# Performance work log

Measured on AMD Instinct MI355X. Metric: run time of the kernel, lower is better.

Reference implementation:

```python
import jax, jax.numpy as jnp
import numpy as np

B, S, H = 8, 2048, 768
VOCAB, MODAL_V, SEG_V, NPI_V, MAX_POS = 32000, 16, 4, 10000, 2048
LN_EPS = 1e-12


def _sinusoidal_table(max_pos, hidden):
    pos = np.arange(max_pos, dtype=np.float32)[:, None]          # [P,1]
    idx = np.arange(hidden, dtype=np.float32)[None, :]           # [1,H]
    angle = pos / np.power(10000.0, 2.0 * idx / hidden)          # even_code/odd_code share 2*idx/H exponent
    tab = np.where(np.arange(hidden)[None, :] % 2 == 0, np.sin(angle), np.cos(angle))
    return jnp.asarray(tab, dtype=jnp.float32)


def setup_inputs() -> dict:
    key = jax.random.key(0)
    ks = jax.random.split(key, 16)
    inp = {
        'word_ids': jax.random.randint(ks[0], (B, S), 0, VOCAB),
        'modalities_ids': jax.random.randint(ks[1], (B, S), 0, MODAL_V),
        'seg_ids': jax.random.randint(ks[2], (B, S), 0, SEG_V),
        'npi_ids': jax.random.randint(ks[3], (B, S), 0, NPI_V),
        'posi_ids': jnp.sort(jax.random.randint(ks[4], (B, S), 0, MAX_POS), axis=-1),
        'age_tau': jax.random.uniform(ks[5], (B, S), dtype=jnp.float32) * 100.0,
        'delays_tau': jax.random.uniform(ks[6], (B, S), dtype=jnp.float32) * 100.0,
        'word_table': jax.random.normal(ks[7], (VOCAB, H), dtype=jnp.float32) * 0.02,
        'modalities_table': jax.random.normal(ks[8], (MODAL_V, H), dtype=jnp.float32) * 0.02,
        'seg_table': jax.random.normal(ks[9], (SEG_V, H), dtype=jnp.float32) * 0.02,
        'npi_table': jax.random.normal(ks[10], (NPI_V, H), dtype=jnp.float32) * 0.02,
        'posi_table': _sinusoidal_table(MAX_POS, H),
        'age_w': jax.random.normal(ks[11], (1, H - 1), dtype=jnp.float32),
        'age_b': jax.random.normal(ks[12], (H - 1,), dtype=jnp.float32),
        'age_w0': jax.random.normal(ks[13], (1, 1), dtype=jnp.float32),
        'age_b0': jax.random.normal(ks[14], (1,), dtype=jnp.float32),
        'delay_w': jax.random.normal(ks[15], (1, H - 1), dtype=jnp.float32),
        'delay_b': jax.random.normal(jax.random.fold_in(key, 100), (H - 1,), dtype=jnp.float32),
        'delay_w0': jax.random.normal(jax.random.fold_in(key, 101), (1, 1), dtype=jnp.float32),
        'delay_b0': jax.random.normal(jax.random.fold_in(key, 102), (1,), dtype=jnp.float32),
        'ln_gamma': jnp.ones((H,), dtype=jnp.float32),
        'ln_beta': jnp.zeros((H,), dtype=jnp.float32),
    }
    return inp


def _time2vec(tau, w, b, w0, b0):
    # tau: [B,S] scalar times; w: [1,H-1]; w0: [1,1]. Vectorized SineActivation.
    t = tau[..., None]                      # [B,S,1]
    v1 = jnp.sin(t * w[0] + b)              # [B,S,H-1]
    v2 = t * w0[0] + b0                     # [B,S,1]
    return jnp.concatenate([v1, v2], axis=-1)


def _layer_norm(x, gamma, beta, eps):
    mu = jnp.mean(x, axis=-1, keepdims=True)
    var = jnp.mean(jnp.square(x - mu), axis=-1, keepdims=True)
    return (x - mu) * jax.lax.rsqrt(var + eps) * gamma + beta


def reference(word_ids, modalities_ids, seg_ids, npi_ids, posi_ids, age_tau, delays_tau,
              word_table, modalities_table, seg_table, npi_table, posi_table,
              age_w, age_b, age_w0, age_b0, delay_w, delay_b, delay_w0, delay_b0,
              ln_gamma, ln_beta):
    word_e = word_table[word_ids]
    seg_e = seg_table[seg_ids]
    modal_e = modalities_table[modalities_ids]
    npi_e = npi_table[npi_ids]
    posi_e = posi_table[posi_ids]
    age_e = _time2vec(age_tau, age_w, age_b, age_w0, age_b0)
    delay_e = _time2vec(delays_tau, delay_w, delay_b, delay_w0, delay_b0)
    # else-branch: sum of all seven embeddings
    emb = word_e + seg_e + posi_e + modal_e + delay_e + age_e + npi_e
    emb = _layer_norm(emb, ln_gamma, ln_beta, LN_EPS)
    return emb  # dropout is identity in eval mode
```

## Files before the change

kernel.cpp:

```cpp
#include <hip/hip_runtime.h>
#include <cmath>

static constexpr int B_ = 8;
static constexpr int S_ = 2048;
static constexpr int H_ = 768;
static constexpr int TOKENS = B_ * S_;
static constexpr float LN_EPS = 1e-12f;

typedef float nfloat4 __attribute__((ext_vector_type(4)));

__device__ __forceinline__ float rfl_f32(float x) {
    return __uint_as_float(__builtin_amdgcn_readfirstlane(__float_as_uint(x)));
}

__global__ __launch_bounds__(256, 5) void bert_emb_kernel(
    const int* __restrict__ word_ids,
    const int* __restrict__ modal_ids,
    const int* __restrict__ seg_ids,
    const int* __restrict__ npi_ids,
    const int* __restrict__ posi_ids,
    const float* __restrict__ age_tau,
    const float* __restrict__ delay_tau,
    const float* __restrict__ word_table,
    const float* __restrict__ modal_table,
    const float* __restrict__ seg_table,
    const float* __restrict__ npi_table,
    const float* __restrict__ posi_table,
    const float* __restrict__ age_w,
    const float* __restrict__ age_b,
    const float* __restrict__ age_w0,
    const float* __restrict__ age_b0,
    const float* __restrict__ delay_w,
    const float* __restrict__ delay_b,
    const float* __restrict__ delay_w0,
    const float* __restrict__ delay_b0,
    const float* __restrict__ ln_gamma,
    const float* __restrict__ ln_beta,
    float* __restrict__ out)
{
    __shared__ __align__(16) float s_aw[H_];
    __shared__ __align__(16) float s_ab[H_];
    __shared__ __align__(16) float s_dw[H_];
    __shared__ __align__(16) float s_db[H_];
    __shared__ __align__(16) float s_g [H_];
    __shared__ __align__(16) float s_bt[H_];

    for (int i = threadIdx.x; i < H_; i += 256) {
        const bool in = (i < H_ - 1);
        s_aw[i] = in ? age_w[i]   : 0.0f;
        s_ab[i] = in ? age_b[i]   : 0.0f;
        s_dw[i] = in ? delay_w[i] : 0.0f;
        s_db[i] = in ? delay_b[i] : 0.0f;
        s_g [i] = ln_gamma[i];
        s_bt[i] = ln_beta[i];
    }
    __syncthreads();

    const int wave = threadIdx.x >> 6;
    const int lane = threadIdx.x & 63;
    const int token = (blockIdx.x << 2) + wave;

    const int wid = __builtin_amdgcn_readfirstlane(word_ids[token]);
    const int mid = __builtin_amdgcn_readfirstlane(modal_ids[token]);
    const int sid = __builtin_amdgcn_readfirstlane(seg_ids[token]);
    const int nid = __builtin_amdgcn_readfirstlane(npi_ids[token]);
    const int pid = __builtin_amdgcn_readfirstlane(posi_ids[token]);
    const float atau = rfl_f32(age_tau[token]);
    const float dtau = rfl_f32(delay_tau[token]);
    const float aw0 = age_w0[0], ab0 = age_b0[0];
    const float dw0 = delay_w0[0], db0 = delay_b0[0];

    const float4* wrow = reinterpret_cast<const float4*>(word_table  + (size_t)wid * H_);
    const float4* mrow = reinterpret_cast<const float4*>(modal_table + (size_t)mid * H_);
    const float4* srow = reinterpret_cast<const float4*>(seg_table   + (size_t)sid * H_);
    const float4* nrow = reinterpret_cast<const float4*>(npi_table   + (size_t)nid * H_);
    const float4* prow = reinterpret_cast<const float4*>(posi_table  + (size_t)pid * H_);

    const float4 w0 = wrow[lane], w1 = wrow[lane + 64], w2 = wrow[lane + 128];
    const float4 m0 = mrow[lane], m1 = mrow[lane + 64], m2 = mrow[lane + 128];
    const float4 s0 = srow[lane], s1 = srow[lane + 64], s2 = srow[lane + 128];
    const float4 n0 = nrow[lane], n1 = nrow[lane + 64], n2 = nrow[lane + 128];
    const float4 p0 = prow[lane], p1 = prow[lane + 64], p2 = prow[lane + 128];

    const float4* awv = reinterpret_cast<const float4*>(s_aw);
    const float4* abv = reinterpret_cast<const float4*>(s_ab);
    const float4* dwv = reinterpret_cast<const float4*>(s_dw);
    const float4* dbv = reinterpret_cast<const float4*>(s_db);

    float vals[12];
    float ssum = 0.0f, ssq = 0.0f;

    const float4 wcs[3] = {w0, w1, w2};
    const float4 mcs[3] = {m0, m1, m2};
    const float4 scs[3] = {s0, s1, s2};
    const float4 ncs[3] = {n0, n1, n2};
    const float4 pcs[3] = {p0, p1, p2};

#pragma unroll
    for (int c = 0; c < 3; ++c) {
        const int h4 = lane + (c << 6);
        const float4 we = wcs[c];
        const float4 me = mcs[c];
        const float4 se = scs[c];
        const float4 ne = ncs[c];
        const float4 pe = pcs[c];

        const float4 aw = awv[h4];
        const float4 ab = abv[h4];
        const float4 dw = dwv[h4];
        const float4 db = dbv[h4];

        float av0 = __sinf(atau * aw.x + ab.x);
        float av1 = __sinf(atau * aw.y + ab.y);
        float av2 = __sinf(atau * aw.z + ab.z);
        float av3 = __sinf(atau * aw.w + ab.w);
        float dv0 = __sinf(dtau * dw.x + db.x);
        float dv1 = __sinf(dtau * dw.y + db.y);
        float dv2 = __sinf(dtau * dw.z + db.z);
        float dv3 = __sinf(dtau * dw.w + db.w);
        if (h4 == (H_ / 4 - 1)) {
            av3 = atau * aw0 + ab0;
            dv3 = dtau * dw0 + db0;
        }

        const float e0 = we.x + me.x + se.x + ne.x + pe.x + av0 + dv0;
        const float e1 = we.y + me.y + se.y + ne.y + pe.y + av1 + dv1;
        const float e2 = we.z + me.z + se.z + ne.z + pe.z + av2 + dv2;
        const float e3 = we.w + me.w + se.w + ne.w + pe.w + av3 + dv3;

        vals[c * 4 + 0] = e0;
        vals[c * 4 + 1] = e1;
        vals[c * 4 + 2] = e2;
        vals[c * 4 + 3] = e3;
        ssum += e0 + e1 + e2 + e3;
        ssq  += e0 * e0 + e1 * e1 + e2 * e2 + e3 * e3;
    }

#pragma unroll
    for (int off = 32; off > 0; off >>= 1) {
        ssum += __shfl_down(ssum, off);
        ssq  += __shfl_down(ssq,  off);
    }
    ssum = __shfl(ssum, 0);
    ssq  = __shfl(ssq,  0);

    const float inv_h = 1.0f / (float)H_;
    const float mu = ssum * inv_h;
    const float var = ssq * inv_h - mu * mu;
    const float rstd = rsqrtf(var + LN_EPS);

    const float4* gv = reinterpret_cast<const float4*>(s_g);
    const float4* bv = reinterpret_cast<const float4*>(s_bt);
    nfloat4* orow = reinterpret_cast<nfloat4*>(out + (size_t)token * H_);

#pragma unroll
    for (int c = 0; c < 3; ++c) {
        const int h4 = lane + (c << 6);
        const float4 g  = gv[h4];
        const float4 bt = bv[h4];
        nfloat4 o;
        o.x = (vals[c * 4 + 0] - mu) * rstd * g.x + bt.x;
        o.y = (vals[c * 4 + 1] - mu) * rstd * g.y + bt.y;
        o.z = (vals[c * 4 + 2] - mu) * rstd * g.z + bt.z;
        o.w = (vals[c * 4 + 3] - mu) * rstd * g.w + bt.w;
        __builtin_nontemporal_store(o, &orow[h4]);
    }
}

extern "C" void kernel_launch(void* const* d_in, const int* in_sizes, int n_in,
                              void* d_out, int out_size, void* d_ws, size_t ws_size,
                              hipStream_t stream) {
    const int*   word_ids    = (const int*)  d_in[0];
    const int*   modal_ids   = (const int*)  d_in[1];
    const int*   seg_ids     = (const int*)  d_in[2];
    const int*   npi_ids     = (const int*)  d_in[3];
    const int*   posi_ids    = (const int*)  d_in[4];
    const float* age_tau     = (const float*)d_in[5];
    const float* delay_tau   = (const float*)d_in[6];
    const float* word_table  = (const float*)d_in[7];
    const float* modal_table = (const float*)d_in[8];
    const float* seg_table   = (const float*)d_in[9];
    const float* npi_table   = (const float*)d_in[10];
    const float* posi_table  = (const float*)d_in[11];
    const float* age_w       = (const float*)d_in[12];
    const float* age_b       = (const float*)d_in[13];
    const float* age_w0      = (const float*)d_in[14];
    const float* age_b0      = (const float*)d_in[15];
    const float* delay_w     = (const float*)d_in[16];
    const float* delay_b     = (const float*)d_in[17];
    const float* delay_w0    = (const float*)d_in[18];
    const float* delay_b0    = (const float*)d_in[19];
    const float* ln_gamma    = (const float*)d_in[20];
    const float* ln_beta     = (const float*)d_in[21];
    float* out = (float*)d_out;

    dim3 grid(TOKENS / 4);
    dim3 block(256);
    hipLaunchKernelGGL(bert_emb_kernel, grid, block, 0, stream,
                       word_ids, modal_ids, seg_ids, npi_ids, posi_ids,
                       age_tau, delay_tau,
                       word_table, modal_table, seg_table, npi_table, posi_table,
                       age_w, age_b, age_w0, age_b0,
                       delay_w, delay_b, delay_w0, delay_b0,
                       ln_gamma, ln_beta, out);
}
```

Measured before the change: 231.2 us.

## Vectorize smem staging, stage gather loads, raise occupancy bound, use xor reduction

Raises the launch-bounds occupancy hint from 5 to 6 blocks per CU. Shared-memory parameter staging now uses one float4 per thread instead of scalar loops. Gathers of the third row chunk are deferred until after the first chunk is consumed, which cuts live registers. The LayerNorm reduction switches to an xor butterfly that removes the final broadcast shuffles. The risk is that fewer loads in flight per wave reduce memory-level parallelism in this bandwidth-bound gather kernel.

```diff
diff --git a/kernel.cpp b/kernel.cpp
--- a/kernel.cpp
+++ b/kernel.cpp
@@ -13,7 +13,7 @@
     return __uint_as_float(__builtin_amdgcn_readfirstlane(__float_as_uint(x)));
 }
 
-__global__ __launch_bounds__(256, 5) void bert_emb_kernel(
+__global__ __launch_bounds__(256, 6) void bert_emb_kernel(
     const int* __restrict__ word_ids,
     const int* __restrict__ modal_ids,
     const int* __restrict__ seg_ids,
@@ -45,14 +45,26 @@
     __shared__ __align__(16) float s_g [H_];
     __shared__ __align__(16) float s_bt[H_];
 
-    for (int i = threadIdx.x; i < H_; i += 256) {
-        const bool in = (i < H_ - 1);
-        s_aw[i] = in ? age_w[i]   : 0.0f;
-        s_ab[i] = in ? age_b[i]   : 0.0f;
-        s_dw[i] = in ? delay_w[i] : 0.0f;
-        s_db[i] = in ? delay_b[i] : 0.0f;
-        s_g [i] = ln_gamma[i];
-        s_bt[i] = ln_beta[i];
+    if (threadIdx.x < 192) {
+        const int i4 = threadIdx.x;
+        float4 vaw, vab, vdw, vdb;
+        if (i4 < 191) {
+            vaw = reinterpret_cast<const float4*>(age_w)[i4];
+            vab = reinterpret_cast<const float4*>(age_b)[i4];
+            vdw = reinterpret_cast<const float4*>(delay_w)[i4];
+            vdb = reinterpret_cast<const float4*>(delay_b)[i4];
+        } else {
+            vaw = make_float4(age_w[764],   age_w[765],   age_w[766],   0.0f);
+            vab = make_float4(age_b[764],   age_b[765],   age_b[766],   0.0f);
+            vdw = make_float4(delay_w[764], delay_w[765], delay_w[766], 0.0f);
+            vdb = make_float4(delay_b[764], delay_b[765], delay_b[766], 0.0f);
+        }
+        reinterpret_cast<float4*>(s_aw)[i4] = vaw;
+        reinterpret_cast<float4*>(s_ab)[i4] = vab;
+        reinterpret_cast<float4*>(s_dw)[i4] = vdw;
+        reinterpret_cast<float4*>(s_db)[i4] = vdb;
+        reinterpret_cast<float4*>(s_g )[i4] = reinterpret_cast<const float4*>(ln_gamma)[i4];
+        reinterpret_cast<float4*>(s_bt)[i4] = reinterpret_cast<const float4*>(ln_beta)[i4];
     }
     __syncthreads();
 
@@ -76,12 +88,6 @@
     const float4* nrow = reinterpret_cast<const float4*>(npi_table   + (size_t)nid * H_);
     const float4* prow = reinterpret_cast<const float4*>(posi_table  + (size_t)pid * H_);
 
-    const float4 w0 = wrow[lane], w1 = wrow[lane + 64], w2 = wrow[lane + 128];
-    const float4 m0 = mrow[lane], m1 = mrow[lane + 64], m2 = mrow[lane + 128];
-    const float4 s0 = srow[lane], s1 = srow[lane + 64], s2 = srow[lane + 128];
-    const float4 n0 = nrow[lane], n1 = nrow[lane + 64], n2 = nrow[lane + 128];
-    const float4 p0 = prow[lane], p1 = prow[lane + 64], p2 = prow[lane + 128];
-
     const float4* awv = reinterpret_cast<const float4*>(s_aw);
     const float4* abv = reinterpret_cast<const float4*>(s_ab);
     const float4* dwv = reinterpret_cast<const float4*>(s_dw);
@@ -90,21 +96,9 @@
     float vals[12];
     float ssum = 0.0f, ssq = 0.0f;
 
-    const float4 wcs[3] = {w0, w1, w2};
-    const float4 mcs[3] = {m0, m1, m2};
-    const float4 scs[3] = {s0, s1, s2};
-    const float4 ncs[3] = {n0, n1, n2};
-    const float4 pcs[3] = {p0, p1, p2};
-
-#pragma unroll
-    for (int c = 0; c < 3; ++c) {
+    auto consume = [&](int c, const float4& we, const float4& me,
+                       const float4& se, const float4& ne, const float4& pe) {
         const int h4 = lane + (c << 6);
-        const float4 we = wcs[c];
-        const float4 me = mcs[c];
-        const float4 se = scs[c];
-        const float4 ne = ncs[c];
-        const float4 pe = pcs[c];
-
         const float4 aw = awv[h4];
         const float4 ab = abv[h4];
         const float4 dw = dwv[h4];
@@ -118,7 +112,7 @@
         float dv1 = __sinf(dtau * dw.y + db.y);
         float dv2 = __sinf(dtau * dw.z + db.z);
         float dv3 = __sinf(dtau * dw.w + db.w);
-        if (h4 == (H_ / 4 - 1)) {
+        if (c == 2 && lane == 63) {
             av3 = atau * aw0 + ab0;
             dv3 = dtau * dw0 + db0;
         }
@@ -134,15 +128,30 @@
         vals[c * 4 + 3] = e3;
         ssum += e0 + e1 + e2 + e3;
         ssq  += e0 * e0 + e1 * e1 + e2 * e2 + e3 * e3;
+    };
+
+    const float4 w0 = wrow[lane], w1 = wrow[lane + 64];
+    const float4 m0 = mrow[lane], m1 = mrow[lane + 64];
+    const float4 s0 = srow[lane], s1 = srow[lane + 64];
+    const float4 n0 = nrow[lane], n1 = nrow[lane + 64];
+    const float4 p0 = prow[lane], p1 = prow[lane + 64];
+
+    consume(0, w0, m0, s0, n0, p0);
+
+    const float4 w2 = wrow[lane + 128];
+    const float4 m2 = mrow[lane + 128];
+    const float4 s2 = srow[lane + 128];
+    const float4 n2 = nrow[lane + 128];
+    const float4 p2 = prow[lane + 128];
+
+    consume(1, w1, m1, s1, n1, p1);
+    consume(2, w2, m2, s2, n2, p2);
+
+#pragma unroll
+    for (int m = 32; m; m >>= 1) {
+        ssum += __shfl_xor(ssum, m);
+        ssq  += __shfl_xor(ssq,  m);
     }
-
-#pragma unroll
-    for (int off = 32; off > 0; off >>= 1) {
-        ssum += __shfl_down(ssum, off);
-        ssq  += __shfl_down(ssq,  off);
-    }
-    ssum = __shfl(ssum, 0);
-    ssq  = __shfl(ssq,  0);
 
     const float inv_h = 1.0f / (float)H_;
     const float mu = ssum * inv_h;
```

After: 231.4 us. Within noise of the previous version (+0.1%).
